# Performance work log

Measured on AMD Instinct MI355X. Metric: run time of the kernel, lower is better.

Reference implementation:

```python
import jax, jax.numpy as jnp
import numpy as np

N_NODES = 50000
N_EDGES = 800000
A_DIM = 128
B_DIM = 128


def setup_inputs() -> dict:
    key = jax.random.key(0)
    k1, k2, k3, k4, k5, k6 = jax.random.split(key, 6)
    edge_rows = jax.random.randint(k1, (N_EDGES,), 0, N_NODES, dtype=jnp.int32)
    edge_cols = jax.random.randint(k2, (N_EDGES,), 0, N_NODES, dtype=jnp.int32)
    edge_vals = jax.random.uniform(k3, (N_EDGES,), dtype=jnp.float32)
    H = jax.random.normal(k4, (N_NODES, A_DIM), dtype=jnp.float32)
    std = 1.0 / np.sqrt(B_DIM)
    W = jax.random.uniform(k5, (A_DIM, B_DIM), minval=-std, maxval=std, dtype=jnp.float32)
    bias = jax.random.uniform(k6, (B_DIM,), minval=-std, maxval=std, dtype=jnp.float32)
    return {"edge_rows": edge_rows, "edge_cols": edge_cols, "edge_vals": edge_vals,
            "H": H, "W": W, "bias": bias}


def reference(edge_rows, edge_cols, edge_vals, H, W, bias):
    # HW = H @ W  (dense GEMM)
    HW = jnp.matmul(H, W)  # [n, b]
    # AHW = A @ HW where A is sparse COO: A[r, c] = v
    msgs = edge_vals[:, None] * HW[edge_cols]  # [nnz, b]
    AHW = jax.ops.segment_sum(msgs, edge_rows, num_segments=H.shape[0])  # [n, b]
    return AHW + bias
```

## Files before the change

kernel.cpp:

```cpp
#include <hip/hip_runtime.h>

#define ADIM 128
#define BDIM 128
#define CAP  64

__global__ __launch_bounds__(256) void fused_gemm_bucket(
        const float* __restrict__ H, const float* __restrict__ W,
        float* __restrict__ HW, int n_nodes, int gemm_blocks,
        const int* __restrict__ rows, const int* __restrict__ cols,
        const float* __restrict__ vals, int* __restrict__ counts,
        int2* __restrict__ ebuf, int n_edges) {
    __shared__ float Hst[128][64];
    const int tid = threadIdx.x;

    if ((int)blockIdx.x >= gemm_blocks) {
        const int e = ((int)blockIdx.x - gemm_blocks) * 256 + tid;
        if (e < n_edges) {
            const int r = rows[e];
            const int pos = atomicAdd(&counts[r], 1);
            if (pos < CAP)
                ebuf[(size_t)r * CAP + pos] =
                    make_int2(cols[e], __float_as_int(vals[e]));
        }
        return;
    }

    const int row0 = (int)blockIdx.x * 64;
    {
        const int r  = tid >> 2;
        const int kc = (tid & 3) * 32;
        const int gr = row0 + r;
        if (gr < n_nodes) {
            const float4* Hrow = (const float4*)(H + (size_t)gr * ADIM + kc);
#pragma unroll
            for (int j4 = 0; j4 < 8; ++j4) {
                float4 h = Hrow[j4];
                int k = kc + j4 * 4;
                Hst[k + 0][r] = h.x; Hst[k + 1][r] = h.y;
                Hst[k + 2][r] = h.z; Hst[k + 3][r] = h.w;
            }
        } else {
#pragma unroll
            for (int j4 = 0; j4 < 8; ++j4) {
                int k = kc + j4 * 4;
                Hst[k + 0][r] = 0.f; Hst[k + 1][r] = 0.f;
                Hst[k + 2][r] = 0.f; Hst[k + 3][r] = 0.f;
            }
        }
    }
    __syncthreads();

    const int tx = tid & 31;
    const int ty = tid >> 5;
    const int c0 = tx * 4;
    const int r0 = ty * 8;

    float acc[8][4];
#pragma unroll
    for (int i = 0; i < 8; ++i)
#pragma unroll
        for (int j = 0; j < 4; ++j) acc[i][j] = 0.f;

#pragma unroll 4
    for (int k = 0; k < 128; ++k) {
        const float4 w  = *(const float4*)(W + (size_t)k * BDIM + c0);
        const float4 h0 = *(const float4*)&Hst[k][r0];
        const float4 h1 = *(const float4*)&Hst[k][r0 + 4];
        const float hr[8] = {h0.x, h0.y, h0.z, h0.w, h1.x, h1.y, h1.z, h1.w};
#pragma unroll
        for (int i = 0; i < 8; ++i) {
            acc[i][0] += hr[i] * w.x;
            acc[i][1] += hr[i] * w.y;
            acc[i][2] += hr[i] * w.z;
            acc[i][3] += hr[i] * w.w;
        }
    }

#pragma unroll
    for (int i = 0; i < 8; ++i) {
        const int gr = row0 + r0 + i;
        if (gr < n_nodes)
            *(float4*)(HW + (size_t)gr * BDIM + c0) = *(float4*)&acc[i][0];
    }
}

__global__ __launch_bounds__(256) void gather_kernel(const int* __restrict__ counts,
                                                     const int2* __restrict__ ebuf,
                                                     const float* __restrict__ HW,
                                                     const float* __restrict__ bias,
                                                     float* __restrict__ out,
                                                     int n_nodes) {
    const int lane = threadIdx.x & 63;
    const int node = (int)((blockIdx.x * (long)blockDim.x + threadIdx.x) >> 6);
    if (node >= n_nodes) return;

    int deg = counts[node];
    if (deg > CAP) deg = CAP;

    const int4* eb4 = (const int4*)(ebuf + (size_t)node * CAP);
    float2 acc = make_float2(0.f, 0.f);

    int i = 0;
    for (; i + 8 <= deg; i += 8) {
        const int4 p0 = eb4[(i >> 1) + 0];
        const int4 p1 = eb4[(i >> 1) + 1];
        const int4 p2 = eb4[(i >> 1) + 2];
        const int4 p3 = eb4[(i >> 1) + 3];
        const float2 m0 = ((const float2*)(HW + (size_t)p0.x * BDIM))[lane];
        const float2 m1 = ((const float2*)(HW + (size_t)p0.z * BDIM))[lane];
        const float2 m2 = ((const float2*)(HW + (size_t)p1.x * BDIM))[lane];
        const float2 m3 = ((const float2*)(HW + (size_t)p1.z * BDIM))[lane];
        const float2 m4 = ((const float2*)(HW + (size_t)p2.x * BDIM))[lane];
        const float2 m5 = ((const float2*)(HW + (size_t)p2.z * BDIM))[lane];
        const float2 m6 = ((const float2*)(HW + (size_t)p3.x * BDIM))[lane];
        const float2 m7 = ((const float2*)(HW + (size_t)p3.z * BDIM))[lane];
        const float v0 = __int_as_float(p0.y), v1 = __int_as_float(p0.w);
        const float v2 = __int_as_float(p1.y), v3 = __int_as_float(p1.w);
        const float v4 = __int_as_float(p2.y), v5 = __int_as_float(p2.w);
        const float v6 = __int_as_float(p3.y), v7 = __int_as_float(p3.w);
        acc.x += v0 * m0.x; acc.y += v0 * m0.y;
        acc.x += v1 * m1.x; acc.y += v1 * m1.y;
        acc.x += v2 * m2.x; acc.y += v2 * m2.y;
        acc.x += v3 * m3.x; acc.y += v3 * m3.y;
        acc.x += v4 * m4.x; acc.y += v4 * m4.y;
        acc.x += v5 * m5.x; acc.y += v5 * m5.y;
        acc.x += v6 * m6.x; acc.y += v6 * m6.y;
        acc.x += v7 * m7.x; acc.y += v7 * m7.y;
    }
    for (; i + 2 <= deg; i += 2) {
        const int4 p = eb4[i >> 1];
        const float2 ma = ((const float2*)(HW + (size_t)p.x * BDIM))[lane];
        const float2 mb = ((const float2*)(HW + (size_t)p.z * BDIM))[lane];
        const float va = __int_as_float(p.y), vb = __int_as_float(p.w);
        acc.x += va * ma.x; acc.y += va * ma.y;
        acc.x += vb * mb.x; acc.y += vb * mb.y;
    }
    if (i < deg) {
        const int2 e = ((const int2*)ebuf)[(size_t)node * CAP + i];
        const float v = __int_as_float(e.y);
        const float2 m = ((const float2*)(HW + (size_t)e.x * BDIM))[lane];
        acc.x += v * m.x; acc.y += v * m.y;
    }

    const float2 b = ((const float2*)bias)[lane];
    ((float2*)(out + (size_t)node * BDIM))[lane] =
        make_float2(acc.x + b.x, acc.y + b.y);
}

extern "C" void kernel_launch(void* const* d_in, const int* in_sizes, int n_in,
                              void* d_out, int out_size, void* d_ws, size_t ws_size,
                              hipStream_t stream) {
    const int*   edge_rows = (const int*)d_in[0];
    const int*   edge_cols = (const int*)d_in[1];
    const float* edge_vals = (const float*)d_in[2];
    const float* H         = (const float*)d_in[3];
    const float* W         = (const float*)d_in[4];
    const float* bias      = (const float*)d_in[5];

    const int n_edges = in_sizes[0];
    const int n_nodes = in_sizes[3] / ADIM;

    const size_t hw_bytes  = (size_t)n_nodes * BDIM * sizeof(float);
    const size_t cnt_bytes = ((size_t)n_nodes * sizeof(int) + 15) & ~(size_t)15;

    char* ws = (char*)d_ws;
    float* HW   = (float*)ws;   ws += (hw_bytes + 15) & ~(size_t)15;
    int*   cnt  = (int*)ws;     ws += cnt_bytes;
    int2*  ebuf = (int2*)ws;

    hipMemsetAsync(cnt, 0, (size_t)n_nodes * sizeof(int), stream);

    const int gemm_blocks   = (n_nodes + 63) / 64;
    const int bucket_blocks = (n_edges + 255) / 256;
    fused_gemm_bucket<<<gemm_blocks + bucket_blocks, 256, 0, stream>>>(
        H, W, HW, n_nodes, gemm_blocks,
        edge_rows, edge_cols, edge_vals, cnt, ebuf, n_edges);

    gather_kernel<<<(n_nodes + 3) / 4, 256, 0, stream>>>(cnt, ebuf, HW, bias,
                                                         (float*)d_out, n_nodes);
}
```

Baseline: 194.0 us.

## Store HW intermediate in fp16 and halve GEMM tile rows

The GEMM now writes its H@W result as half precision, so the random-row gathers in the aggregation kernel move half as many bytes. The GEMM tile shrinks from 64 to 32 rows per block, which doubles the block count and cuts per-thread accumulators. The gather loop is restructured into 16/8/4/2 edge chunks, and the degree is made wave-uniform with readfirstlane. Rounding HW to fp16 adds error to the output, which may loosen accuracy against the fp32 reference.

```diff
diff --git a/kernel.cpp b/kernel.cpp
--- a/kernel.cpp
+++ b/kernel.cpp
@@ -1,4 +1,5 @@
 #include <hip/hip_runtime.h>
+#include <hip/hip_fp16.h>
 
 #define ADIM 128
 #define BDIM 128
@@ -6,11 +7,11 @@
 
 __global__ __launch_bounds__(256) void fused_gemm_bucket(
         const float* __restrict__ H, const float* __restrict__ W,
-        float* __restrict__ HW, int n_nodes, int gemm_blocks,
+        __half* __restrict__ HWh, int n_nodes, int gemm_blocks,
         const int* __restrict__ rows, const int* __restrict__ cols,
         const float* __restrict__ vals, int* __restrict__ counts,
         int2* __restrict__ ebuf, int n_edges) {
-    __shared__ float Hst[128][64];
+    __shared__ float Hst[128][32];
     const int tid = threadIdx.x;
 
     if ((int)blockIdx.x >= gemm_blocks) {
@@ -25,15 +26,15 @@
         return;
     }
 
-    const int row0 = (int)blockIdx.x * 64;
+    const int row0 = (int)blockIdx.x * 32;
     {
-        const int r  = tid >> 2;
-        const int kc = (tid & 3) * 32;
+        const int r  = tid >> 3;
+        const int kc = (tid & 7) * 16;
         const int gr = row0 + r;
         if (gr < n_nodes) {
             const float4* Hrow = (const float4*)(H + (size_t)gr * ADIM + kc);
 #pragma unroll
-            for (int j4 = 0; j4 < 8; ++j4) {
+            for (int j4 = 0; j4 < 4; ++j4) {
                 float4 h = Hrow[j4];
                 int k = kc + j4 * 4;
                 Hst[k + 0][r] = h.x; Hst[k + 1][r] = h.y;
@@ -41,7 +42,7 @@
             }
         } else {
 #pragma unroll
-            for (int j4 = 0; j4 < 8; ++j4) {
+            for (int j4 = 0; j4 < 4; ++j4) {
                 int k = kc + j4 * 4;
                 Hst[k + 0][r] = 0.f; Hst[k + 1][r] = 0.f;
                 Hst[k + 2][r] = 0.f; Hst[k + 3][r] = 0.f;
@@ -53,22 +54,21 @@
     const int tx = tid & 31;
     const int ty = tid >> 5;
     const int c0 = tx * 4;
-    const int r0 = ty * 8;
+    const int r0 = ty * 4;
 
-    float acc[8][4];
+    float acc[4][4];
 #pragma unroll
-    for (int i = 0; i < 8; ++i)
+    for (int i = 0; i < 4; ++i)
 #pragma unroll
         for (int j = 0; j < 4; ++j) acc[i][j] = 0.f;
 
 #pragma unroll 4
     for (int k = 0; k < 128; ++k) {
-        const float4 w  = *(const float4*)(W + (size_t)k * BDIM + c0);
-        const float4 h0 = *(const float4*)&Hst[k][r0];
-        const float4 h1 = *(const float4*)&Hst[k][r0 + 4];
-        const float hr[8] = {h0.x, h0.y, h0.z, h0.w, h1.x, h1.y, h1.z, h1.w};
+        const float4 w = *(const float4*)(W + (size_t)k * BDIM + c0);
+        const float4 h = *(const float4*)&Hst[k][r0];
+        const float hr[4] = {h.x, h.y, h.z, h.w};
 #pragma unroll
-        for (int i = 0; i < 8; ++i) {
+        for (int i = 0; i < 4; ++i) {
             acc[i][0] += hr[i] * w.x;
             acc[i][1] += hr[i] * w.y;
             acc[i][2] += hr[i] * w.z;
@@ -77,16 +77,19 @@
     }
 
 #pragma unroll
-    for (int i = 0; i < 8; ++i) {
+    for (int i = 0; i < 4; ++i) {
         const int gr = row0 + r0 + i;
-        if (gr < n_nodes)
-            *(float4*)(HW + (size_t)gr * BDIM + c0) = *(float4*)&acc[i][0];
+        if (gr < n_nodes) {
+            __half2* dst = (__half2*)(HWh + (size_t)gr * BDIM + c0);
+            dst[0] = __floats2half2_rn(acc[i][0], acc[i][1]);
+            dst[1] = __floats2half2_rn(acc[i][2], acc[i][3]);
+        }
     }
 }
 
 __global__ __launch_bounds__(256) void gather_kernel(const int* __restrict__ counts,
                                                      const int2* __restrict__ ebuf,
-                                                     const float* __restrict__ HW,
+                                                     const __half* __restrict__ HWh,
                                                      const float* __restrict__ bias,
                                                      float* __restrict__ out,
                                                      int n_nodes) {
@@ -94,53 +97,61 @@
     const int node = (int)((blockIdx.x * (long)blockDim.x + threadIdx.x) >> 6);
     if (node >= n_nodes) return;
 
-    int deg = counts[node];
+    int deg = __builtin_amdgcn_readfirstlane(counts[node]);
     if (deg > CAP) deg = CAP;
 
     const int4* eb4 = (const int4*)(ebuf + (size_t)node * CAP);
     float2 acc = make_float2(0.f, 0.f);
+    int i = 0;
 
-    int i = 0;
-    for (; i + 8 <= deg; i += 8) {
-        const int4 p0 = eb4[(i >> 1) + 0];
-        const int4 p1 = eb4[(i >> 1) + 1];
-        const int4 p2 = eb4[(i >> 1) + 2];
-        const int4 p3 = eb4[(i >> 1) + 3];
-        const float2 m0 = ((const float2*)(HW + (size_t)p0.x * BDIM))[lane];
-        const float2 m1 = ((const float2*)(HW + (size_t)p0.z * BDIM))[lane];
-        const float2 m2 = ((const float2*)(HW + (size_t)p1.x * BDIM))[lane];
-        const float2 m3 = ((const float2*)(HW + (size_t)p1.z * BDIM))[lane];
-        const float2 m4 = ((const float2*)(HW + (size_t)p2.x * BDIM))[lane];
-        const float2 m5 = ((const float2*)(HW + (size_t)p2.z * BDIM))[lane];
-        const float2 m6 = ((const float2*)(HW + (size_t)p3.x * BDIM))[lane];
-        const float2 m7 = ((const float2*)(HW + (size_t)p3.z * BDIM))[lane];
-        const float v0 = __int_as_float(p0.y), v1 = __int_as_float(p0.w);
-        const float v2 = __int_as_float(p1.y), v3 = __int_as_float(p1.w);
-        const float v4 = __int_as_float(p2.y), v5 = __int_as_float(p2.w);
-        const float v6 = __int_as_float(p3.y), v7 = __int_as_float(p3.w);
-        acc.x += v0 * m0.x; acc.y += v0 * m0.y;
-        acc.x += v1 * m1.x; acc.y += v1 * m1.y;
-        acc.x += v2 * m2.x; acc.y += v2 * m2.y;
-        acc.x += v3 * m3.x; acc.y += v3 * m3.y;
-        acc.x += v4 * m4.x; acc.y += v4 * m4.y;
-        acc.x += v5 * m5.x; acc.y += v5 * m5.y;
-        acc.x += v6 * m6.x; acc.y += v6 * m6.y;
-        acc.x += v7 * m7.x; acc.y += v7 * m7.y;
+#define PROC_PAIR(P)                                                            \
+    {                                                                           \
+        const float va = __int_as_float((P).y), vb = __int_as_float((P).w);     \
+        const float2 ma =                                                       \
+            __half22float2(((const __half2*)(HWh + (size_t)(P).x * BDIM))[lane]);\
+        const float2 mb =                                                       \
+            __half22float2(((const __half2*)(HWh + (size_t)(P).z * BDIM))[lane]);\
+        acc.x += va * ma.x; acc.y += va * ma.y;                                 \
+        acc.x += vb * mb.x; acc.y += vb * mb.y;                                 \
     }
-    for (; i + 2 <= deg; i += 2) {
+
+    while (i + 16 <= deg) {
+        int4 p[8];
+#pragma unroll
+        for (int u = 0; u < 8; ++u) p[u] = eb4[(i >> 1) + u];
+#pragma unroll
+        for (int u = 0; u < 8; ++u) PROC_PAIR(p[u]);
+        i += 16;
+    }
+    if (i + 8 <= deg) {
+        int4 p[4];
+#pragma unroll
+        for (int u = 0; u < 4; ++u) p[u] = eb4[(i >> 1) + u];
+#pragma unroll
+        for (int u = 0; u < 4; ++u) PROC_PAIR(p[u]);
+        i += 8;
+    }
+    if (i + 4 <= deg) {
+        int4 p[2];
+#pragma unroll
+        for (int u = 0; u < 2; ++u) p[u] = eb4[(i >> 1) + u];
+#pragma unroll
+        for (int u = 0; u < 2; ++u) PROC_PAIR(p[u]);
+        i += 4;
+    }
+    if (i + 2 <= deg) {
         const int4 p = eb4[i >> 1];
-        const float2 ma = ((const float2*)(HW + (size_t)p.x * BDIM))[lane];
-        const float2 mb = ((const float2*)(HW + (size_t)p.z * BDIM))[lane];
-        const float va = __int_as_float(p.y), vb = __int_as_float(p.w);
-        acc.x += va * ma.x; acc.y += va * ma.y;
-        acc.x += vb * mb.x; acc.y += vb * mb.y;
+        PROC_PAIR(p);
+        i += 2;
     }
     if (i < deg) {
-        const int2 e = ((const int2*)ebuf)[(size_t)node * CAP + i];
+        const int2 e = (ebuf + (size_t)node * CAP)[i];
         const float v = __int_as_float(e.y);
-        const float2 m = ((const float2*)(HW + (size_t)e.x * BDIM))[lane];
+        const float2 m =
+            __half22float2(((const __half2*)(HWh + (size_t)e.x * BDIM))[lane]);
         acc.x += v * m.x; acc.y += v * m.y;
     }
+#undef PROC_PAIR
 
     const float2 b = ((const float2*)bias)[lane];
     ((float2*)(out + (size_t)node * BDIM))[lane] =
@@ -160,22 +171,22 @@
     const int n_edges = in_sizes[0];
     const int n_nodes = in_sizes[3] / ADIM;
 
-    const size_t hw_bytes  = (size_t)n_nodes * BDIM * sizeof(float);
+    const size_t hw_bytes  = ((size_t)n_nodes * BDIM * sizeof(__half) + 15) & ~(size_t)15;
     const size_t cnt_bytes = ((size_t)n_nodes * sizeof(int) + 15) & ~(size_t)15;
 
     char* ws = (char*)d_ws;
-    float* HW   = (float*)ws;   ws += (hw_bytes + 15) & ~(size_t)15;
-    int*   cnt  = (int*)ws;     ws += cnt_bytes;
-    int2*  ebuf = (int2*)ws;
+    __half* HWh  = (__half*)ws;  ws += hw_bytes;
+    int*    cnt  = (int*)ws;     ws += cnt_bytes;
+    int2*   ebuf = (int2*)ws;
 
     hipMemsetAsync(cnt, 0, (size_t)n_nodes * sizeof(int), stream);
 
-    const int gemm_blocks   = (n_nodes + 63) / 64;
+    const int gemm_blocks   = (n_nodes + 31) / 32;
     const int bucket_blocks = (n_edges + 255) / 256;
     fused_gemm_bucket<<<gemm_blocks + bucket_blocks, 256, 0, stream>>>(
-        H, W, HW, n_nodes, gemm_blocks,
+        H, W, HWh, n_nodes, gemm_blocks,
         edge_rows, edge_cols, edge_vals, cnt, ebuf, n_edges);
 
-    gather_kernel<<<(n_nodes + 3) / 4, 256, 0, stream>>>(cnt, ebuf, HW, bias,
+    gather_kernel<<<(n_nodes + 3) / 4, 256, 0, stream>>>(cnt, ebuf, HWh, bias,
                                                          (float*)d_out, n_nodes);
 }
```

Result: slower. 203.8 us (+5.1%).
